# Kernel tuning notes

Measured on AMD Instinct MI355X. Metric: run time of the kernel, lower is better.

The kernel has to match this reference:

```python
import jax, jax.numpy as jnp
import numpy as np

B, Q, D, H, CTX, W_OUT = 2048, 256, 64, 128, 5, 32


def setup_inputs() -> dict:
    key = jax.random.key(0)
    ks = jax.random.split(key, 20)
    s = 0.05
    p = lambda k, shape: jax.random.normal(k, shape, dtype=jnp.float32) * s
    return {
        "x_in": jax.random.normal(ks[0], (B, Q, D), dtype=jnp.float32),
        "w_out": W_OUT,
        "conv_w": p(ks[1], (H, 3 * D, CTX)),
        "conv_b": p(ks[2], (H,)),
        "fc1_w": p(ks[3], (H, H)),
        "fc1_b": p(ks[4], (H,)),
        "fc2_w": p(ks[5], (D, H)),
        "fc2_b": p(ks[6], (D,)),
        "rot1_w": p(ks[7], (H, D)),
        "rot1_b": p(ks[8], (H,)),
        "rot2_w": p(ks[9], (2, H)),
        "rot2_b": p(ks[10], (2,)),
        "gru_wih": p(ks[11], (3 * H, D)),
        "gru_whh": p(ks[12], (3 * H, H)),
        "gru_bih": p(ks[13], (3 * H,)),
        "gru_bhh": p(ks[14], (3 * H,)),
        "out_w": p(ks[15], (D, H)),
        "out_b": p(ks[16], (D,)),
    }


def reference(x_in, w_out, conv_w, conv_b, fc1_w, fc1_b, fc2_w, fc2_b,
              rot1_w, rot1_b, rot2_w, rot2_b, gru_wih, gru_whh,
              gru_bih, gru_bhh, out_w, out_b):
    b, q, d = x_in.shape
    h_dim = fc1_w.shape[0]
    ctx = conv_w.shape[2]
    m = d // 2
    pi = np.float32(np.pi)

    def kalman_step(carry, y_t):
        x_post, y_prev, buf = carry
        # rotation params from posterior state
        rp = jnp.maximum(x_post @ rot1_w.T + rot1_b, 0.0) @ rot2_w.T + rot2_b
        rho = jax.nn.sigmoid(rp[:, 0:1]) * 1.5
        phi = jnp.tanh(rp[:, 1:2]) * pi
        # complex polar rotation: (a+ib) * rho*e^{i phi}
        a, bb = x_post[:, :m], x_post[:, m:]
        c = rho * jnp.cos(phi)
        s = rho * jnp.sin(phi)
        x_pri = jnp.concatenate([a * c - bb * s, a * s + bb * c], axis=1)
        innov = y_t - x_pri
        diff = y_t - y_prev
        feat = jnp.concatenate([innov, x_post, diff], axis=1)  # (B, 3D)
        # roll context buffer, append newest features
        buf = jnp.concatenate([buf[:, :, 1:], feat[:, :, None]], axis=2)
        # Conv1d(kernel=context, pad=0) over a context-length buffer == full contraction
        t = jnp.einsum('hck,bck->bh', conv_w, buf) + conv_b
        t = jnp.maximum(t, 0.0)
        t = jnp.maximum(t @ fc1_w.T + fc1_b, 0.0)
        K = jax.nn.sigmoid(t @ fc2_w.T + fc2_b)  # (B, D)
        x_post_new = x_pri + K * innov
        return (x_post_new, y_t, buf), None

    init = (jnp.zeros((b, d), x_in.dtype),
            x_in[:, 0, :],
            jnp.zeros((b, 3 * d, ctx), x_in.dtype))
    (x_post, _, _), _ = jax.lax.scan(kalman_step, init, jnp.swapaxes(x_in, 0, 1))

    def gru_step(carry, _):
        h, curr = carry
        gi = curr @ gru_wih.T + gru_bih
        gh = h @ gru_whh.T + gru_bhh
        i_r, i_z, i_n = jnp.split(gi, 3, axis=1)
        h_r, h_z, h_n = jnp.split(gh, 3, axis=1)
        r = jax.nn.sigmoid(i_r + h_r)
        z = jax.nn.sigmoid(i_z + h_z)
        n = jnp.tanh(i_n + r * h_n)
        h_new = (1.0 - z) * n + z * h
        curr_new = curr + (h_new @ out_w.T + out_b)
        return (h_new, curr_new), curr_new

    (_, _), preds = jax.lax.scan(
        gru_step, (jnp.zeros((b, h_dim), x_in.dtype), x_post), None, length=w_out)
    return jnp.swapaxes(preds, 0, 1)  # (B, w_out, D)
```

## Files before the change

kernel.cpp:

```cpp
#include <hip/hip_runtime.h>

#define QLEN 256
#define DDIM 64
#define WOUT 32

typedef __bf16 b8v __attribute__((ext_vector_type(8)));
typedef float f4v __attribute__((ext_vector_type(4)));

__device__ __forceinline__ f4v MFMA(b8v a, b8v b, f4v c) {
  return __builtin_amdgcn_mfma_f32_16x16x32_bf16(a, b, c, 0, 0, 0);
}
__device__ __forceinline__ float sigmoidf_(float x) { return 1.0f/(1.0f+__expf(-x)); }
__device__ __forceinline__ float tanhf_(float x)    { return 1.0f - 2.0f/(__expf(2.0f*x)+1.0f); }

__global__ __launch_bounds__(512, 2)
void k_kalman(const float* __restrict__ x_in,
              const float* __restrict__ conv_w, const float* __restrict__ conv_b,
              const float* __restrict__ fc1_w,  const float* __restrict__ fc1_b,
              const float* __restrict__ fc2_w,  const float* __restrict__ fc2_b,
              const float* __restrict__ rot1_w, const float* __restrict__ rot1_b,
              const float* __restrict__ rot2_w, const float* __restrict__ rot2_b,
              float* __restrict__ out)
{
  __shared__ __align__(16) __bf16 SMB[24064];
  __shared__ __align__(16) float  SMF[3584];
  const int tid = threadIdx.x;
  const int w  = tid >> 6;
  const int l  = tid & 63;
  const int lr = l & 15;
  const int lg = l >> 4;
  const int wg = blockIdx.x;
  const bool lo = (w < 4);

  __bf16* XPB  = SMB;
  __bf16* T1   = SMB + 1152;
  __bf16* TC   = SMB + 3456;
  __bf16* T2   = SMB + 5760;
  __bf16* FEAT = SMB + 8064;
  float*  XPF  = SMF;
  float*  XPRI = SMF + 512;
  float*  INV  = SMF + 1024;
  float*  PART = SMF + 1536;

  for (int i = tid; i < 24064; i += 512) SMB[i] = (__bf16)0.0f;
  for (int i = tid; i < 3584;  i += 512) SMF[i] = 0.0f;

  const int hcol = 16*w + lr;
  const int tlo  = 2*(w & 3);

  b8v r1B[2], f1B[4], f2B[4], cvB[15][2];
  #pragma unroll
  for (int q = 0; q < 2; ++q)
    #pragma unroll
    for (int j = 0; j < 8; ++j)
      r1B[q][j] = (__bf16)rot1_w[hcol*64 + q*32 + lg*8 + j];
  #pragma unroll
  for (int q = 0; q < 4; ++q)
    #pragma unroll
    for (int j = 0; j < 8; ++j)
      f1B[q][j] = (__bf16)fc1_w[hcol*128 + q*32 + lg*8 + j];
  {
    const int h2 = lo ? hcol : 0;
    #pragma unroll
    for (int q = 0; q < 4; ++q)
      #pragma unroll
      for (int j = 0; j < 8; ++j)
        f2B[q][j] = (__bf16)fc2_w[h2*128 + q*32 + lg*8 + j];
  }
  #pragma unroll
  for (int i = 0; i < 15; ++i) {
    const int f = lo ? ((i < 9) ? (6+i) : (i-9)) : (15+i);
    const int L = f/6, q = f%6;
    #pragma unroll
    for (int ti = 0; ti < 2; ++ti)
      #pragma unroll
      for (int j = 0; j < 8; ++j)
        cvB[i][ti][j] =
          (__bf16)conv_w[((tlo+ti)*16 + lr)*960 + (q*32 + lg*8 + j)*5 + (4-L)];
  }

  const float b_r1 = rot1_b[hcol];
  const float b_f1 = fc1_b[hcol];
  const float b_f2 = fc2_b[lo ? hcol : 0];
  const float bc0  = conv_b[tlo*16 + lr];
  const float bc1  = conv_b[(tlo+1)*16 + lr];
  const float r2w00 = rot2_w[l],       r2w01 = rot2_w[64 + l];
  const float r2w10 = rot2_w[128 + l], r2w11 = rot2_w[192 + l];
  const float rb0 = rot2_b[0], rb1 = rot2_b[1];
  const float PI_F = 3.14159274f;

  const float* xptr = x_in + ((long)(wg*8 + w)*QLEN)*DDIM + l;
  float y_cur = xptr[0];
  float y_prv = y_cur;
  int slot = 0;

  __syncthreads();

  for (int t = 0; t < QLEN; ++t) {
    {
      b8v a0 = *(const b8v*)&XPB[lr*72      + lg*8];
      b8v a1 = *(const b8v*)&XPB[lr*72 + 32 + lg*8];
      f4v C = {};
      C = MFMA(a0, r1B[0], C);
      C = MFMA(a1, r1B[1], C);
      #pragma unroll
      for (int r = 0; r < 4; ++r) {
        float v = C[r] + b_r1; v = v > 0.f ? v : 0.f;
        T1[(lg*4+r)*144 + hcol] = (__bf16)v;
      }
    }
    __syncthreads();

    f4v C0a = {}, C0b = {}, C1a = {}, C1b = {};
    if (lo) {
      #pragma unroll
      for (int i = 0; i < 9; ++i) {
        const int f = 6+i, L = f/6, q = f%6;
        int s5 = slot - L; if (s5 < 0) s5 += 5;
        b8v a = *(const b8v*)&FEAT[s5*3200 + lr*200 + q*32 + lg*8];
        if (i & 1) { C0b = MFMA(a, cvB[i][0], C0b); C1b = MFMA(a, cvB[i][1], C1b); }
        else       { C0a = MFMA(a, cvB[i][0], C0a); C1a = MFMA(a, cvB[i][1], C1a); }
      }
    } else {
      #pragma unroll
      for (int i = 0; i < 15; ++i) {
        const int f = 15+i, L = f/6, q = f%6;
        int s5 = slot - L; if (s5 < 0) s5 += 5;
        b8v a = *(const b8v*)&FEAT[s5*3200 + lr*200 + q*32 + lg*8];
        if (i & 1) { C0b = MFMA(a, cvB[i][0], C0b); C1b = MFMA(a, cvB[i][1], C1b); }
        else       { C0a = MFMA(a, cvB[i][0], C0a); C1a = MFMA(a, cvB[i][1], C1a); }
      }
    }
    float y_nxt;
    {
      float t1a = (float)T1[w*144 + l];
      float t1b = (float)T1[w*144 + 64 + l];
      float acc0 = t1a*r2w00 + t1b*r2w01;
      float acc1 = t1a*r2w10 + t1b*r2w11;
      #pragma unroll
      for (int m = 1; m < 64; m <<= 1) {
        acc0 += __shfl_xor(acc0, m, 64);
        acc1 += __shfl_xor(acc1, m, 64);
      }
      float rho = 1.5f * sigmoidf_(acc0 + rb0);
      float phi = PI_F * tanhf_(acc1 + rb1);
      float cc = rho * __cosf(phi);
      float ss = rho * __sinf(phi);
      float lo32 = XPF[w*64 + (l & 31)];
      float hi32 = XPF[w*64 + (l & 31) + 32];
      float xpri = (l < 32) ? (lo32*cc - hi32*ss) : (lo32*ss + hi32*cc);
      float innov = y_cur - xpri;
      float diff  = y_cur - y_prv;
      __bf16* fr = FEAT + slot*3200 + w*200;
      fr[l]       = (__bf16)innov;
      fr[128 + l] = (__bf16)diff;
      XPRI[w*64 + l] = xpri;
      INV [w*64 + l] = innov;
      y_nxt = (t+1 < QLEN) ? xptr[(t+1)*DDIM] : y_cur;
    }
    if (!lo) {
      *(f4v*)&PART[(tlo*16 + lr)*16 + 4*lg]     = C0a + C0b;
      *(f4v*)&PART[((tlo+1)*16 + lr)*16 + 4*lg] = C1a + C1b;
    }
    __syncthreads();

    if (lo) {
      #pragma unroll
      for (int i = 9; i < 15; ++i) {
        const int q = i - 9;
        b8v a = *(const b8v*)&FEAT[slot*3200 + lr*200 + q*32 + lg*8];
        if (i & 1) { C0b = MFMA(a, cvB[i][0], C0b); C1b = MFMA(a, cvB[i][1], C1b); }
        else       { C0a = MFMA(a, cvB[i][0], C0a); C1a = MFMA(a, cvB[i][1], C1a); }
      }
      f4v p0 = *(const f4v*)&PART[(tlo*16 + lr)*16 + 4*lg];
      f4v p1 = *(const f4v*)&PART[((tlo+1)*16 + lr)*16 + 4*lg];
      #pragma unroll
      for (int r = 0; r < 4; ++r) {
        float v0 = C0a[r] + C0b[r] + p0[r] + bc0; v0 = v0 > 0.f ? v0 : 0.f;
        float v1 = C1a[r] + C1b[r] + p1[r] + bc1; v1 = v1 > 0.f ? v1 : 0.f;
        TC[(lg*4+r)*144 + tlo*16 + lr]     = (__bf16)v0;
        TC[(lg*4+r)*144 + (tlo+1)*16 + lr] = (__bf16)v1;
      }
    }
    __syncthreads();

    {
      f4v D0 = {}, D1 = {};
      #pragma unroll
      for (int q = 0; q < 4; ++q) {
        b8v a = *(const b8v*)&TC[lr*144 + q*32 + lg*8];
        if (q & 1) D1 = MFMA(a, f1B[q], D1); else D0 = MFMA(a, f1B[q], D0);
      }
      #pragma unroll
      for (int r = 0; r < 4; ++r) {
        float v = D0[r] + D1[r] + b_f1; v = v > 0.f ? v : 0.f;
        T2[(lg*4+r)*144 + hcol] = (__bf16)v;
      }
    }
    __syncthreads();

    const int slot_next = (slot == 4) ? 0 : slot + 1;
    if (lo) {
      f4v D0 = {}, D1 = {};
      #pragma unroll
      for (int q = 0; q < 4; ++q) {
        b8v a = *(const b8v*)&T2[lr*144 + q*32 + lg*8];
        if (q & 1) D1 = MFMA(a, f2B[q], D1); else D0 = MFMA(a, f2B[q], D0);
      }
      if (lg < 2) {
        #pragma unroll
        for (int r = 0; r < 4; ++r) {
          int e = lg*4 + r;
          float K = sigmoidf_(D0[r] + D1[r] + b_f2);
          float xn = XPRI[e*64 + hcol] + K * INV[e*64 + hcol];
          XPF[e*64 + hcol] = xn;
          XPB[e*72 + hcol] = (__bf16)xn;
          FEAT[slot_next*3200 + e*200 + 64 + hcol] = (__bf16)xn;
        }
      }
    }
    __syncthreads();

    y_prv = y_cur; y_cur = y_nxt;
    slot = slot_next;
  }

  out[((long)(wg*8 + w)*WOUT)*DDIM + l] = XPF[w*64 + l];
}

__global__ __launch_bounds__(512, 2)
void k_gru(const float* __restrict__ gru_wih, const float* __restrict__ gru_whh,
           const float* __restrict__ gru_bih, const float* __restrict__ gru_bhh,
           const float* __restrict__ out_w,   const float* __restrict__ out_b,
           float* __restrict__ out)
{
  __shared__ __align__(16) __bf16 CUR[16*72];
  __shared__ __align__(16) __bf16 HB [16*144];
  const int tid = threadIdx.x;
  const int w  = tid >> 6, l = tid & 63, lr = l & 15, lg = l >> 4;
  const int g = blockIdx.x;

  for (int i = tid; i < 16*144; i += 512) HB[i] = (__bf16)0.f;
  for (int i = tid; i < 16*64; i += 512) {
    int e = i >> 6, d = i & 63;
    CUR[e*72 + d] = (__bf16)out[((long)(g*16 + e)*WOUT)*DDIM + d];
  }

  b8v fih[3][2], fhh[3][4], fo[4];
  #pragma unroll
  for (int n3 = 0; n3 < 3; ++n3) {
    int row = 16*(w + 8*n3) + lr;
    #pragma unroll
    for (int q = 0; q < 2; ++q)
      #pragma unroll
      for (int j = 0; j < 8; ++j)
        fih[n3][q][j] = (__bf16)gru_wih[row*64 + q*32 + lg*8 + j];
    #pragma unroll
    for (int q = 0; q < 4; ++q)
      #pragma unroll
      for (int j = 0; j < 8; ++j)
        fhh[n3][q][j] = (__bf16)gru_whh[row*128 + q*32 + lg*8 + j];
  }
  {
    int row = 16*(w & 3) + lr;
    #pragma unroll
    for (int q = 0; q < 4; ++q)
      #pragma unroll
      for (int j = 0; j < 8; ++j)
        fo[q][j] = (__bf16)out_w[row*128 + q*32 + lg*8 + j];
  }
  const int jh = 16*w + lr;
  const float b_ir = gru_bih[jh], b_iz = gru_bih[128+jh], b_in = gru_bih[256+jh];
  const float b_hr = gru_bhh[jh], b_hz = gru_bhh[128+jh], b_hn = gru_bhh[256+jh];
  const float b_o  = out_b[16*(w & 3) + lr];
  const int dcol = 16*(w & 3) + lr;
  __syncthreads();

  for (int s = 0; s < WOUT; ++s) {
    f4v cI[3] = {}, cH[3] = {};
    #pragma unroll
    for (int q = 0; q < 2; ++q) {
      b8v a = *(const b8v*)&CUR[lr*72 + q*32 + lg*8];
      #pragma unroll
      for (int n3 = 0; n3 < 3; ++n3) cI[n3] = MFMA(a, fih[n3][q], cI[n3]);
    }
    #pragma unroll
    for (int q = 0; q < 4; ++q) {
      b8v a = *(const b8v*)&HB[lr*144 + q*32 + lg*8];
      #pragma unroll
      for (int n3 = 0; n3 < 3; ++n3) cH[n3] = MFMA(a, fhh[n3][q], cH[n3]);
    }
    __syncthreads();

    #pragma unroll
    for (int r = 0; r < 4; ++r) {
      int e = lg*4 + r;
      float ir = cI[0][r] + b_ir, iz = cI[1][r] + b_iz, in_ = cI[2][r] + b_in;
      float hr = cH[0][r] + b_hr, hz = cH[1][r] + b_hz, hn  = cH[2][r] + b_hn;
      float rr = sigmoidf_(ir + hr);
      float zz = sigmoidf_(iz + hz);
      float nn = tanhf_(in_ + rr*hn);
      float hold = (float)HB[e*144 + jh];
      float hnew = (1.f - zz)*nn + zz*hold;
      HB[e*144 + jh] = (__bf16)hnew;
    }
    __syncthreads();

    if (w < 4) {
      f4v C0 = {};
      #pragma unroll
      for (int q = 0; q < 4; ++q) {
        b8v a = *(const b8v*)&HB[lr*144 + q*32 + lg*8];
        C0 = MFMA(a, fo[q], C0);
      }
      #pragma unroll
      for (int r = 0; r < 4; ++r) {
        int e = lg*4 + r;
        float cn = (float)CUR[e*72 + dcol] + C0[r] + b_o;
        CUR[e*72 + dcol] = (__bf16)cn;
        out[(((long)(g*16 + e))*WOUT + s)*DDIM + dcol] = cn;
      }
    }
    __syncthreads();
  }
}

extern "C" void kernel_launch(void* const* d_in, const int* in_sizes, int n_in,
                              void* d_out, int out_size, void* d_ws, size_t ws_size,
                              hipStream_t stream) {
  (void)in_sizes; (void)n_in; (void)d_ws; (void)ws_size; (void)out_size;
  const float* x_in   = (const float*)d_in[0];
  const float* conv_w = (const float*)d_in[2];
  const float* conv_b = (const float*)d_in[3];
  const float* fc1_w  = (const float*)d_in[4];
  const float* fc1_b  = (const float*)d_in[5];
  const float* fc2_w  = (const float*)d_in[6];
  const float* fc2_b  = (const float*)d_in[7];
  const float* rot1_w = (const float*)d_in[8];
  const float* rot1_b = (const float*)d_in[9];
  const float* rot2_w = (const float*)d_in[10];
  const float* rot2_b = (const float*)d_in[11];
  const float* gwih   = (const float*)d_in[12];
  const float* gwhh   = (const float*)d_in[13];
  const float* gbih   = (const float*)d_in[14];
  const float* gbhh   = (const float*)d_in[15];
  const float* ow     = (const float*)d_in[16];
  const float* ob     = (const float*)d_in[17];
  float* out = (float*)d_out;

  k_kalman<<<256, 512, 0, stream>>>(x_in, conv_w, conv_b, fc1_w, fc1_b,
                                    fc2_w, fc2_b, rot1_w, rot1_b,
                                    rot2_w, rot2_b, out);
  k_gru<<<128, 512, 0, stream>>>(gwih, gwhh, gbih, gbhh, ow, ob, out);
}
```

Baseline: 692.6 us.

## Shrink Kalman LDS to 8 live rows, rebalance conv chunks between wave halves

The Kalman kernel only holds 8 batch rows per block, so the padded 16-row MFMA tiles now read a shared zero vector for rows 8-15 and only store the valid half of the outputs. This roughly halves LDS size (FEAT slot stride, T1/TC/T2 strides), which could allow more blocks per CU. The conv chunk split between the low and high wave halves is rebalanced so the low waves do more of the work before the mid-step barrier. The x_in prefetch is hoisted earlier, and the GRU hidden-state buffer stride changes to 136, which may alter LDS bank conflicts.

```diff
diff --git a/kernel.cpp b/kernel.cpp
--- a/kernel.cpp
+++ b/kernel.cpp
@@ -12,6 +12,9 @@
 }
 __device__ __forceinline__ float sigmoidf_(float x) { return 1.0f/(1.0f+__expf(-x)); }
 __device__ __forceinline__ float tanhf_(float x)    { return 1.0f - 2.0f/(__expf(2.0f*x)+1.0f); }
+__device__ __forceinline__ b8v lda(const __bf16* p, const __bf16* zp, bool pr) {
+  return *(const b8v*)(pr ? p : zp);
+}
 
 __global__ __launch_bounds__(512, 2)
 void k_kalman(const float* __restrict__ x_in,
@@ -22,31 +25,35 @@
               const float* __restrict__ rot2_w, const float* __restrict__ rot2_b,
               float* __restrict__ out)
 {
-  __shared__ __align__(16) __bf16 SMB[24064];
-  __shared__ __align__(16) float  SMF[3584];
+  __shared__ __align__(16) __bf16 SMB[11872];
+  __shared__ __align__(16) float  SMF[2560];
   const int tid = threadIdx.x;
   const int w  = tid >> 6;
   const int l  = tid & 63;
   const int lr = l & 15;
   const int lg = l >> 4;
   const int wg = blockIdx.x;
-  const bool lo = (w < 4);
+  const bool lo  = (w < 4);
+  const bool pr8 = (lr < 8);
 
   __bf16* XPB  = SMB;
-  __bf16* T1   = SMB + 1152;
-  __bf16* TC   = SMB + 3456;
-  __bf16* T2   = SMB + 5760;
-  __bf16* FEAT = SMB + 8064;
+  __bf16* T1   = SMB + 576;
+  __bf16* TC   = SMB + 1664;
+  __bf16* T2   = SMB + 2752;
+  __bf16* FEAT = SMB + 3840;
+  const __bf16* ZP = SMB + 11840;
   float*  XPF  = SMF;
   float*  XPRI = SMF + 512;
   float*  INV  = SMF + 1024;
   float*  PART = SMF + 1536;
 
-  for (int i = tid; i < 24064; i += 512) SMB[i] = (__bf16)0.0f;
-  for (int i = tid; i < 3584;  i += 512) SMF[i] = 0.0f;
+  for (int i = tid; i < 11872; i += 512) SMB[i] = (__bf16)0.0f;
+  for (int i = tid; i < 2560;  i += 512) SMF[i] = 0.0f;
 
   const int hcol = 16*w + lr;
   const int tlo  = 2*(w & 3);
+
+  constexpr int LO_CH[15] = {2,3,6,7,8,9,10,11,12,13,14, 0,1,4,5};
 
   b8v r1B[2], f1B[4], f2B[4], cvB[15][2];
   #pragma unroll
@@ -69,8 +76,8 @@
   }
   #pragma unroll
   for (int i = 0; i < 15; ++i) {
-    const int f = lo ? ((i < 9) ? (6+i) : (i-9)) : (15+i);
-    const int L = f/6, q = f%6;
+    const int c = lo ? LO_CH[i] : (15 + i);
+    const int L = c/6, q = c%6;
     #pragma unroll
     for (int ti = 0; ti < 2; ++ti)
       #pragma unroll
@@ -98,43 +105,45 @@
 
   for (int t = 0; t < QLEN; ++t) {
     {
-      b8v a0 = *(const b8v*)&XPB[lr*72      + lg*8];
-      b8v a1 = *(const b8v*)&XPB[lr*72 + 32 + lg*8];
+      b8v a0 = lda(&XPB[lr*72      + lg*8], ZP, pr8);
+      b8v a1 = lda(&XPB[lr*72 + 32 + lg*8], ZP, pr8);
       f4v C = {};
       C = MFMA(a0, r1B[0], C);
       C = MFMA(a1, r1B[1], C);
-      #pragma unroll
-      for (int r = 0; r < 4; ++r) {
-        float v = C[r] + b_r1; v = v > 0.f ? v : 0.f;
-        T1[(lg*4+r)*144 + hcol] = (__bf16)v;
-      }
-    }
-    __syncthreads();
-
+      if (lg < 2) {
+        #pragma unroll
+        for (int r = 0; r < 4; ++r) {
+          float v = C[r] + b_r1; v = v > 0.f ? v : 0.f;
+          T1[(lg*4+r)*136 + hcol] = (__bf16)v;
+        }
+      }
+    }
+    __syncthreads();
+
+    float t1a = (float)T1[w*136 + l];
+    float t1b = (float)T1[w*136 + 64 + l];
+    float y_nxt = (t+1 < QLEN) ? xptr[(t+1)*DDIM] : y_cur;
     f4v C0a = {}, C0b = {}, C1a = {}, C1b = {};
     if (lo) {
       #pragma unroll
-      for (int i = 0; i < 9; ++i) {
-        const int f = 6+i, L = f/6, q = f%6;
+      for (int i = 0; i < 11; ++i) {
+        const int c = LO_CH[i], L = c/6, q = c%6;
         int s5 = slot - L; if (s5 < 0) s5 += 5;
-        b8v a = *(const b8v*)&FEAT[s5*3200 + lr*200 + q*32 + lg*8];
+        b8v a = lda(&FEAT[s5*1600 + lr*200 + q*32 + lg*8], ZP, pr8);
         if (i & 1) { C0b = MFMA(a, cvB[i][0], C0b); C1b = MFMA(a, cvB[i][1], C1b); }
         else       { C0a = MFMA(a, cvB[i][0], C0a); C1a = MFMA(a, cvB[i][1], C1a); }
       }
     } else {
       #pragma unroll
       for (int i = 0; i < 15; ++i) {
-        const int f = 15+i, L = f/6, q = f%6;
+        const int c = 15+i, L = c/6, q = c%6;
         int s5 = slot - L; if (s5 < 0) s5 += 5;
-        b8v a = *(const b8v*)&FEAT[s5*3200 + lr*200 + q*32 + lg*8];
+        b8v a = lda(&FEAT[s5*1600 + lr*200 + q*32 + lg*8], ZP, pr8);
         if (i & 1) { C0b = MFMA(a, cvB[i][0], C0b); C1b = MFMA(a, cvB[i][1], C1b); }
         else       { C0a = MFMA(a, cvB[i][0], C0a); C1a = MFMA(a, cvB[i][1], C1a); }
       }
     }
-    float y_nxt;
     {
-      float t1a = (float)T1[w*144 + l];
-      float t1b = (float)T1[w*144 + 64 + l];
       float acc0 = t1a*r2w00 + t1b*r2w01;
       float acc1 = t1a*r2w10 + t1b*r2w11;
       #pragma unroll
@@ -151,35 +160,37 @@
       float xpri = (l < 32) ? (lo32*cc - hi32*ss) : (lo32*ss + hi32*cc);
       float innov = y_cur - xpri;
       float diff  = y_cur - y_prv;
-      __bf16* fr = FEAT + slot*3200 + w*200;
+      __bf16* fr = FEAT + slot*1600 + w*200;
       fr[l]       = (__bf16)innov;
       fr[128 + l] = (__bf16)diff;
       XPRI[w*64 + l] = xpri;
       INV [w*64 + l] = innov;
-      y_nxt = (t+1 < QLEN) ? xptr[(t+1)*DDIM] : y_cur;
-    }
-    if (!lo) {
-      *(f4v*)&PART[(tlo*16 + lr)*16 + 4*lg]     = C0a + C0b;
-      *(f4v*)&PART[((tlo+1)*16 + lr)*16 + 4*lg] = C1a + C1b;
+    }
+    if (!lo && lg < 2) {
+      f4v s0 = C0a + C0b, s1 = C1a + C1b;
+      *(f4v*)&PART[tlo*128     + lr*8 + lg*4] = s0;
+      *(f4v*)&PART[(tlo+1)*128 + lr*8 + lg*4] = s1;
     }
     __syncthreads();
 
     if (lo) {
       #pragma unroll
-      for (int i = 9; i < 15; ++i) {
-        const int q = i - 9;
-        b8v a = *(const b8v*)&FEAT[slot*3200 + lr*200 + q*32 + lg*8];
+      for (int i = 11; i < 15; ++i) {
+        const int q = LO_CH[i] % 6;
+        b8v a = lda(&FEAT[slot*1600 + lr*200 + q*32 + lg*8], ZP, pr8);
         if (i & 1) { C0b = MFMA(a, cvB[i][0], C0b); C1b = MFMA(a, cvB[i][1], C1b); }
         else       { C0a = MFMA(a, cvB[i][0], C0a); C1a = MFMA(a, cvB[i][1], C1a); }
       }
-      f4v p0 = *(const f4v*)&PART[(tlo*16 + lr)*16 + 4*lg];
-      f4v p1 = *(const f4v*)&PART[((tlo+1)*16 + lr)*16 + 4*lg];
-      #pragma unroll
-      for (int r = 0; r < 4; ++r) {
-        float v0 = C0a[r] + C0b[r] + p0[r] + bc0; v0 = v0 > 0.f ? v0 : 0.f;
-        float v1 = C1a[r] + C1b[r] + p1[r] + bc1; v1 = v1 > 0.f ? v1 : 0.f;
-        TC[(lg*4+r)*144 + tlo*16 + lr]     = (__bf16)v0;
-        TC[(lg*4+r)*144 + (tlo+1)*16 + lr] = (__bf16)v1;
+      if (lg < 2) {
+        f4v p0 = *(const f4v*)&PART[tlo*128     + lr*8 + lg*4];
+        f4v p1 = *(const f4v*)&PART[(tlo+1)*128 + lr*8 + lg*4];
+        #pragma unroll
+        for (int r = 0; r < 4; ++r) {
+          float v0 = C0a[r] + C0b[r] + p0[r] + bc0; v0 = v0 > 0.f ? v0 : 0.f;
+          float v1 = C1a[r] + C1b[r] + p1[r] + bc1; v1 = v1 > 0.f ? v1 : 0.f;
+          TC[(lg*4+r)*136 + tlo*16 + lr]     = (__bf16)v0;
+          TC[(lg*4+r)*136 + (tlo+1)*16 + lr] = (__bf16)v1;
+        }
       }
     }
     __syncthreads();
@@ -188,13 +199,15 @@
       f4v D0 = {}, D1 = {};
       #pragma unroll
       for (int q = 0; q < 4; ++q) {
-        b8v a = *(const b8v*)&TC[lr*144 + q*32 + lg*8];
+        b8v a = lda(&TC[lr*136 + q*32 + lg*8], ZP, pr8);
         if (q & 1) D1 = MFMA(a, f1B[q], D1); else D0 = MFMA(a, f1B[q], D0);
       }
-      #pragma unroll
-      for (int r = 0; r < 4; ++r) {
-        float v = D0[r] + D1[r] + b_f1; v = v > 0.f ? v : 0.f;
-        T2[(lg*4+r)*144 + hcol] = (__bf16)v;
+      if (lg < 2) {
+        #pragma unroll
+        for (int r = 0; r < 4; ++r) {
+          float v = D0[r] + D1[r] + b_f1; v = v > 0.f ? v : 0.f;
+          T2[(lg*4+r)*136 + hcol] = (__bf16)v;
+        }
       }
     }
     __syncthreads();
@@ -204,7 +217,7 @@
       f4v D0 = {}, D1 = {};
       #pragma unroll
       for (int q = 0; q < 4; ++q) {
-        b8v a = *(const b8v*)&T2[lr*144 + q*32 + lg*8];
+        b8v a = lda(&T2[lr*136 + q*32 + lg*8], ZP, pr8);
         if (q & 1) D1 = MFMA(a, f2B[q], D1); else D0 = MFMA(a, f2B[q], D0);
       }
       if (lg < 2) {
@@ -215,7 +228,7 @@
           float xn = XPRI[e*64 + hcol] + K * INV[e*64 + hcol];
           XPF[e*64 + hcol] = xn;
           XPB[e*72 + hcol] = (__bf16)xn;
-          FEAT[slot_next*3200 + e*200 + 64 + hcol] = (__bf16)xn;
+          FEAT[slot_next*1600 + e*200 + 64 + hcol] = (__bf16)xn;
         }
       }
     }
@@ -235,12 +248,12 @@
            float* __restrict__ out)
 {
   __shared__ __align__(16) __bf16 CUR[16*72];
-  __shared__ __align__(16) __bf16 HB [16*144];
+  __shared__ __align__(16) __bf16 HB [16*136];
   const int tid = threadIdx.x;
   const int w  = tid >> 6, l = tid & 63, lr = l & 15, lg = l >> 4;
   const int g = blockIdx.x;
 
-  for (int i = tid; i < 16*144; i += 512) HB[i] = (__bf16)0.f;
+  for (int i = tid; i < 16*136; i += 512) HB[i] = (__bf16)0.f;
   for (int i = tid; i < 16*64; i += 512) {
     int e = i >> 6, d = i & 63;
     CUR[e*72 + d] = (__bf16)out[((long)(g*16 + e)*WOUT)*DDIM + d];
@@ -286,7 +299,7 @@
     }
     #pragma unroll
     for (int q = 0; q < 4; ++q) {
-      b8v a = *(const b8v*)&HB[lr*144 + q*32 + lg*8];
+      b8v a = *(const b8v*)&HB[lr*136 + q*32 + lg*8];
       #pragma unroll
       for (int n3 = 0; n3 < 3; ++n3) cH[n3] = MFMA(a, fhh[n3][q], cH[n3]);
     }
@@ -300,9 +313,9 @@
       float rr = sigmoidf_(ir + hr);
       float zz = sigmoidf_(iz + hz);
       float nn = tanhf_(in_ + rr*hn);
-      float hold = (float)HB[e*144 + jh];
+      float hold = (float)HB[e*136 + jh];
       float hnew = (1.f - zz)*nn + zz*hold;
-      HB[e*144 + jh] = (__bf16)hnew;
+      HB[e*136 + jh] = (__bf16)hnew;
     }
     __syncthreads();
 
@@ -310,7 +323,7 @@
       f4v C0 = {};
       #pragma unroll
       for (int q = 0; q < 4; ++q) {
-        b8v a = *(const b8v*)&HB[lr*144 + q*32 + lg*8];
+        b8v a = *(const b8v*)&HB[lr*136 + q*32 + lg*8];
         C0 = MFMA(a, fo[q], C0);
       }
       #pragma unroll
```

Measured after the change: 737.9 us. 6.5% more time.
